# Performance work log

Hardware: AMD Instinct MI355X
Metric: run time of the kernel (lower is better)

Reference implementation:

```python
import jax, jax.numpy as jnp
import numpy as np

C = 2048
EPS = 1e-12


def conv1x1(x, w, b):
    # x: [B,C_in,H,W], w: [C_out,C_in], b: [C_out]
    return jnp.einsum('oc,bchw->bohw', w, x) + b[None, :, None, None]


def unfold3x3(x):
    # torch F.unfold(kernel=3, padding=1): output [B, C*9, H*W],
    # feature order (c, ki, kj) with c slowest.
    B, Cc, H, W = x.shape
    xp = jnp.pad(x, ((0, 0), (0, 0), (1, 1), (1, 1)))
    patches = jnp.stack([xp[:, :, ki:ki + H, kj:kj + W]
                         for ki in range(3) for kj in range(3)], axis=2)  # [B,C,9,H,W]
    return patches.reshape(B, Cc * 9, H * W)


def fold3x3(u, H, W):
    # torch F.fold(kernel=3, padding=1): overlap-add. u: [B, C*9, H*W]
    B = u.shape[0]
    Cc = u.shape[1] // 9
    t = u.reshape(B, Cc, 3, 3, H, W)
    out = jnp.zeros((B, Cc, H + 2, W + 2), dtype=u.dtype)
    for ki in range(3):
        for kj in range(3):
            out = out.at[:, :, ki:ki + H, kj:kj + W].add(t[:, :, ki, kj])
    return out[:, :, 1:1 + H, 1:1 + W]


def l2norm(x, axis):
    n = jnp.sqrt(jnp.sum(x * x, axis=axis, keepdims=True))
    return x / jnp.maximum(n, EPS)


def setup_inputs() -> dict:
    key = jax.random.key(0)
    ks = jax.random.split(key, 8)
    B, H, W = 4, 24, 24
    s = 0.02
    return {
        'part_ref': jax.random.normal(ks[0], (B, C, H, W), jnp.float32),
        'part_target': jax.random.normal(ks[1], (B, C, H, W), jnp.float32),
        'wq': jax.random.normal(ks[2], (C, C), jnp.float32) * s,
        'bq': jnp.zeros((C,), jnp.float32),
        'wk': jax.random.normal(ks[3], (C, C), jnp.float32) * s,
        'bk': jnp.zeros((C,), jnp.float32),
        'wt': jax.random.normal(ks[4], (C, 2 * C), jnp.float32) * s,
        'bt': jnp.zeros((C,), jnp.float32),
    }


def reference(part_ref, part_target, wq, bq, wk, bk, wt, bt):
    B, _, H, W = part_ref.shape
    part_target_o = part_target
    k = conv1x1(part_ref, wk, bk)
    q = conv1x1(part_target, wq, bq)

    tgt_unf = unfold3x3(q)        # [B, C*9, L]
    ref_unf1 = unfold3x3(k)       # [B, C*9, L]

    ref_n = l2norm(jnp.transpose(ref_unf1, (0, 2, 1)), axis=2)  # [B, L, C*9]
    tgt_n = l2norm(tgt_unf, axis=1)                              # [B, C*9, L]

    R = jnp.einsum('blc,bcm->blm', ref_n, tgt_n)  # [B, L_ref, L_tgt]
    R_star = jnp.max(R, axis=1)                   # [B, L]
    R_arg = jnp.argmax(R, axis=1)                 # [B, L]

    # gather best ref patch per target location along dim 2
    T_unf = jnp.take_along_axis(ref_unf1, R_arg[:, None, :], axis=2)  # [B, C*9, L]
    T_part = fold3x3(T_unf, H, W) / 9.0

    S = R_star.reshape(B, 1, H, W)
    x_res = jnp.concatenate((q, T_part), axis=1)  # [B, 2C, H, W]
    res = conv1x1(x_res, wt, bt) * S + part_target_o
    return res
```

## Files before the change

### kernel.cpp

```cpp
#include <hip/hip_runtime.h>
#include <cstddef>
#include <cstdint>

#define LPIX 576
#define CCH  2048
#define NB   4

typedef __attribute__((ext_vector_type(8))) short short8;
typedef __attribute__((ext_vector_type(4))) float f32x4;
typedef __attribute__((ext_vector_type(4))) unsigned short u16x4;

__device__ __forceinline__ unsigned short f2bf(float f) {
    uint32_t u = __builtin_bit_cast(uint32_t, f);
    u += 0x7fff + ((u >> 16) & 1);
    return (unsigned short)(u >> 16);
}
__device__ __forceinline__ float bf2f(unsigned short s) {
    return __builtin_bit_cast(float, (uint32_t)s << 16);
}

__device__ __forceinline__ void gload_lds16(const void* g, void* l) {
    __builtin_amdgcn_global_load_lds((const __attribute__((address_space(1))) void*)g,
                                     (__attribute__((address_space(3))) void*)l, 16, 0, 0);
}

template<int BM, int BN>
__device__ __forceinline__ void mm_core64(
    const short* __restrict__ Ab, int lda,
    const short* __restrict__ Bb, int ldb,
    int k0, int kend, short* As, short* Bs,
    int m0, int n0, f32x4 (&acc)[BM/32][BN/32])
{
    const int tid  = threadIdx.x;
    const int lane = tid & 63;
    const int w    = tid >> 6;
    const int wm = (w & 1) * (BM / 2);
    const int wn = (w >> 1) * (BN / 2);
    const int l15 = lane & 15;
    const int k8  = (lane >> 4) * 8;
    const int r   = tid >> 2;
    const int kk  = (tid & 3) * 8;

    const short* Aptr[BM / 32]; short* Alds[BM / 32];
    #pragma unroll
    for (int u = 0; u < BM / 32; ++u) {
        const int p = u & 1, g = u >> 1;
        Aptr[u] = Ab + (size_t)(m0 + g * 64 + r) * lda + p * 32 + kk;
        Alds[u] = As + p * BM * 32 + g * 2048 + tid * 8;
    }
    const short* Bptr[BN / 32]; short* Blds[BN / 32];
    #pragma unroll
    for (int u = 0; u < BN / 32; ++u) {
        const int p = u & 1, g = u >> 1;
        Bptr[u] = Bb + (size_t)(n0 + g * 64 + r) * ldb + p * 32 + kk;
        Blds[u] = Bs + p * BN * 32 + g * 2048 + tid * 8;
    }

    for (int c0 = k0; c0 < kend; c0 += 64) {
        #pragma unroll
        for (int u = 0; u < BM / 32; ++u) gload_lds16(Aptr[u] + c0, Alds[u]);
        #pragma unroll
        for (int u = 0; u < BN / 32; ++u) gload_lds16(Bptr[u] + c0, Blds[u]);
        __syncthreads();
        #pragma unroll
        for (int s = 0; s < 2; ++s) {
            short8 fa[BM / 32], fb[BN / 32];
            #pragma unroll
            for (int i = 0; i < BM / 32; ++i)
                fa[i] = *(const short8*)(As + s * BM * 32 + (wm + i * 16 + l15) * 32 + k8);
            #pragma unroll
            for (int j = 0; j < BN / 32; ++j)
                fb[j] = *(const short8*)(Bs + s * BN * 32 + (wn + j * 16 + l15) * 32 + k8);
            #pragma unroll
            for (int i = 0; i < BM / 32; ++i)
                #pragma unroll
                for (int j = 0; j < BN / 32; ++j)
                    acc[i][j] = __builtin_amdgcn_mfma_f32_16x16x32_bf16(fa[i], fb[j], acc[i][j], 0, 0, 0);
        }
        __syncthreads();
    }
}

__global__ __launch_bounds__(256) void wcast2_k(const float* __restrict__ wq,
                                                const float* __restrict__ wk,
                                                short* __restrict__ Wb) {
    const float* W = blockIdx.y ? wk : wq;
    short* D = Wb + (size_t)blockIdx.y * CCH * CCH;
    int i = (blockIdx.x * 256 + threadIdx.x) * 4;
    float4 v = *(const float4*)(W + i);
    u16x4 u;
    u.x = f2bf(v.x); u.y = f2bf(v.y); u.z = f2bf(v.z); u.w = f2bf(v.w);
    *(u16x4*)(D + i) = u;
}

__global__ __launch_bounds__(256) void wcast_k(const float* __restrict__ W,
                                               short* __restrict__ Wb) {
    int i = (blockIdx.x * 256 + threadIdx.x) * 4;
    float4 v = *(const float4*)(W + i);
    u16x4 u;
    u.x = f2bf(v.x); u.y = f2bf(v.y); u.z = f2bf(v.z); u.w = f2bf(v.w);
    *(u16x4*)(Wb + i) = u;
}

__global__ __launch_bounds__(256) void tcast_k(const float* __restrict__ tgt,
                                               const float* __restrict__ ref,
                                               short* __restrict__ T1) {
    __shared__ float tile[32][33];
    const int z = blockIdx.z;
    const int b = z & 3, which = z >> 2;
    const float* X = (which ? ref : tgt) + (size_t)b * CCH * LPIX;
    const int c0 = blockIdx.y * 32;
    const int l0 = blockIdx.x * 32;
    const int tx = threadIdx.x, ty = threadIdx.y;
    #pragma unroll
    for (int j = 0; j < 4; ++j)
        tile[ty + j * 8][tx] = X[(size_t)(c0 + ty + j * 8) * LPIX + l0 + tx];
    __syncthreads();
    short* D = T1 + ((size_t)(which * NB + b) * LPIX) * CCH;
    #pragma unroll
    for (int j = 0; j < 4; ++j)
        D[(size_t)(l0 + ty + j * 8) * CCH + c0 + tx] = (short)f2bf(tile[tx][ty + j * 8]);
}

__global__ __launch_bounds__(256) void conv_k(
    const short* __restrict__ T1, const short* __restrict__ Wb,
    const float* __restrict__ bq, const float* __restrict__ bk,
    short* __restrict__ x2t, short* __restrict__ kt,
    float* __restrict__ nq, float* __restrict__ nk)
{
    __shared__ short As[64 * 64];
    __shared__ short Bs[128 * 64];
    const int id = blockIdx.x;
    const int xcd = id & 7, slot = id >> 3;
    const int sid = xcd * 4 + slot / 36;
    const int r36 = slot % 36;
    const int which = sid >> 4;
    const int m0 = (r36 % 9) * 64;
    const int n0 = (sid & 15) * 128;
    const int b  = r36 / 9;
    const short* Ab = T1 + (size_t)(which * NB + b) * LPIX * CCH;
    const short* Bb = Wb + (size_t)which * CCH * CCH;
    const float* bias = which ? bk : bq;
    short* Yb = which ? (kt + (size_t)b * LPIX * CCH) : (x2t + (size_t)b * LPIX * 4096);
    float* Nb = (which ? nk : nq) + b * LPIX;
    const int ldy = which ? CCH : 4096;
    f32x4 acc[2][4] = {};
    mm_core64<64, 128>(Ab, CCH, Bb, CCH, 0, CCH, As, Bs, m0, n0, acc);
    const int lane = threadIdx.x & 63, w = threadIdx.x >> 6;
    const int wm = (w & 1) * 32, wn = (w >> 1) * 64;
    const int l15 = lane & 15, quad = lane >> 4;
    float pv[2][4] = {};
    #pragma unroll
    for (int i = 0; i < 2; ++i)
        #pragma unroll
        for (int j = 0; j < 4; ++j) {
            const int gn = n0 + wn + j * 16 + l15;
            const float bi = bias[gn];
            #pragma unroll
            for (int r = 0; r < 4; ++r) {
                const int gm = m0 + wm + i * 16 + quad * 4 + r;
                float v = acc[i][j][r] + bi;
                pv[i][r] += v * v;
                Yb[(size_t)gm * ldy + gn] = (short)f2bf(v);
            }
        }
    #pragma unroll
    for (int i = 0; i < 2; ++i)
        #pragma unroll
        for (int r = 0; r < 4; ++r) {
            float s = pv[i][r];
            #pragma unroll
            for (int m = 1; m < 16; m <<= 1) s += __shfl_xor(s, m);
            if (l15 == 0) {
                const int gm = m0 + wm + i * 16 + quad * 4 + r;
                atomicAdd(&Nb[gm], s);
            }
        }
}

__global__ __launch_bounds__(256) void gram_k(
    const short* __restrict__ kt, const short* __restrict__ x2t,
    float* __restrict__ Mpart)
{
    __shared__ short As[64 * 64];
    __shared__ short Bs[64 * 64];
    const int z = blockIdx.z;
    const int b = z >> 1, kc = z & 1;
    const short* Ab = kt + (size_t)b * LPIX * CCH;
    const short* Bb = x2t + (size_t)b * LPIX * 4096;
    const int m0 = blockIdx.y * 64;
    const int n0 = blockIdx.x * 64;
    f32x4 acc[2][2] = {};
    mm_core64<64, 64>(Ab, CCH, Bb, 4096, kc * 1024, kc * 1024 + 1024, As, Bs, m0, n0, acc);
    float* Mb = Mpart + (size_t)(kc * NB + b) * LPIX * LPIX;
    const int lane = threadIdx.x & 63, w = threadIdx.x >> 6;
    const int wm = (w & 1) * 32, wn = (w >> 1) * 32;
    const int l15 = lane & 15, quad = lane >> 4;
    #pragma unroll
    for (int i = 0; i < 2; ++i)
        #pragma unroll
        for (int j = 0; j < 2; ++j) {
            const int gn = n0 + wn + j * 16 + l15;
            #pragma unroll
            for (int r = 0; r < 4; ++r) {
                const int gm = m0 + wm + i * 16 + quad * 4 + r;
                Mb[(size_t)gm * LPIX + gn] = acc[i][j][r];
            }
        }
}

__global__ __launch_bounds__(256) void fin_k(
    const short* __restrict__ wtb, const short* __restrict__ x2t,
    const float* __restrict__ bt, const float* __restrict__ S,
    const float* __restrict__ PT, float* __restrict__ out)
{
    __shared__ short As[128 * 64];
    __shared__ short Bs[64 * 64];
    const int id = blockIdx.x;
    const int xcd = id & 7, slot = id >> 3;
    const int hi = slot >= 36;
    const int r36 = slot - hi * 36;
    const int m0 = (xcd * 2 + hi) * 128;
    const int n0 = (r36 % 9) * 64;
    const int b  = r36 / 9;
    const short* Bb = x2t + (size_t)b * LPIX * 4096;
    f32x4 acc[4][2] = {};
    mm_core64<128, 64>(wtb, 4096, Bb, 4096, 0, 4096, As, Bs, m0, n0, acc);
    const int lane = threadIdx.x & 63, w = threadIdx.x >> 6;
    const int wm = (w & 1) * 64, wn = (w >> 1) * 32;
    const int l15 = lane & 15, quad = lane >> 4;
    #pragma unroll
    for (int i = 0; i < 4; ++i)
        #pragma unroll
        for (int j = 0; j < 2; ++j) {
            const int gn = n0 + wn + j * 16 + l15;
            const float sv = S[b * LPIX + gn];
            #pragma unroll
            for (int r = 0; r < 4; ++r) {
                const int gm = m0 + wm + i * 16 + quad * 4 + r;
                float v = (acc[i][j][r] + bt[gm]) * sv
                        + PT[((size_t)b * CCH + gm) * LPIX + gn];
                out[((size_t)b * CCH + gm) * LPIX + gn] = v;
            }
        }
}

__global__ __launch_bounds__(256) void argmax1_k(
    const float* __restrict__ Mpart, const float* __restrict__ nk,
    float* __restrict__ Pv, int* __restrict__ Pi)
{
    const int b   = blockIdx.z;
    const int lrb = blockIdx.y;
    const int tx = threadIdx.x, ty = threadIdx.y;
    const int tid = ty * 64 + tx;
    __shared__ float invNkS[24];
    if (tid < 24) {
        const int jr = tid;
        float s = 0.f;
        #pragma unroll
        for (int di = -1; di <= 1; ++di) {
            const int ii = lrb + di;
            if ((unsigned)ii > 23u) continue;
            #pragma unroll
            for (int dj = -1; dj <= 1; ++dj) {
                const int jj = jr + dj;
                if ((unsigned)jj > 23u) continue;
                s += nk[b * LPIX + ii * 24 + jj];
            }
        }
        invNkS[jr] = 1.0f / fmaxf(sqrtf(s), 1e-12f);
    }
    __syncthreads();
    const int lt = blockIdx.x * 64 + tx;
    const int it = lt / 24, jt = lt % 24;
    const float* Mb0 = Mpart + (size_t)b * LPIX * LPIX;
    const float* Mb1 = Mpart + (size_t)(NB + b) * LPIX * LPIX;
    float best = -1e30f; int bidx = 0;
    #pragma unroll
    for (int i = 0; i < 6; ++i) {
        const int jr = ty + i * 4;
        const int lr = lrb * 24 + jr;
        const int base = lr * LPIX + lt;
        float g = 0.f;
        #pragma unroll
        for (int di = -1; di <= 1; ++di) {
            if ((unsigned)(lrb + di) > 23u || (unsigned)(it + di) > 23u) continue;
            #pragma unroll
            for (int dj = -1; dj <= 1; ++dj) {
                if ((unsigned)(jr + dj) > 23u || (unsigned)(jt + dj) > 23u) continue;
                const int o = base + (di * 24 + dj) * (LPIX + 1);
                g += Mb0[o] + Mb1[o];
            }
        }
        float v = g * invNkS[jr];
        if (v > best) { best = v; bidx = lr; }
    }
    __shared__ float rv[4][64];
    __shared__ int   ri[4][64];
    rv[ty][tx] = best; ri[ty][tx] = bidx;
    __syncthreads();
    if (ty == 0) {
        #pragma unroll
        for (int y = 1; y < 4; ++y) {
            float v = rv[y][tx]; int id = ri[y][tx];
            if (v > best || (v == best && id < bidx)) { best = v; bidx = id; }
        }
        Pv[((size_t)b * 24 + lrb) * LPIX + lt] = best;
        Pi[((size_t)b * 24 + lrb) * LPIX + lt] = bidx;
    }
}

__global__ __launch_bounds__(256) void argmax2_k(
    const float* __restrict__ Pv, const int* __restrict__ Pi,
    const float* __restrict__ nq,
    float* __restrict__ S, int* __restrict__ Arg)
{
    int idx = blockIdx.x * 256 + threadIdx.x;
    if (idx >= NB * LPIX) return;
    int b = idx / LPIX, lt = idx % LPIX;
    int it = lt / 24, jt = lt % 24;
    float s = 0.f;
    #pragma unroll
    for (int di = -1; di <= 1; ++di) {
        const int ii = it + di;
        if ((unsigned)ii > 23u) continue;
        #pragma unroll
        for (int dj = -1; dj <= 1; ++dj) {
            const int jj = jt + dj;
            if ((unsigned)jj > 23u) continue;
            s += nq[b * LPIX + ii * 24 + jj];
        }
    }
    const float invNq = 1.0f / fmaxf(sqrtf(s), 1e-12f);
    float best = -1e30f; int bidx = 0;
    #pragma unroll
    for (int c = 0; c < 24; ++c) {
        float v = Pv[((size_t)b * 24 + c) * LPIX + lt];
        int  id = Pi[((size_t)b * 24 + c) * LPIX + lt];
        if (v > best || (v == best && id < bidx)) { best = v; bidx = id; }
    }
    S[idx]   = best * invNq;
    Arg[idx] = bidx;
}

__global__ __launch_bounds__(256) void gather_k(
    const short* __restrict__ kt, const int* __restrict__ Arg,
    short* __restrict__ x2t)
{
    const int id = blockIdx.x;
    const int xcd = id & 7, slot = id >> 3;
    const int b  = xcd >> 1;
    const int l0 = ((xcd & 1) * 72 + slot) * 4;
    const int lane = threadIdx.x, ty = threadIdx.y;
    const int tid = ty * 64 + lane;
    __shared__ int tap[4][9];
    if (tid < 36) {
        int px = tid / 9, t9 = tid % 9;
        int l = l0 + px;
        int i = l / 24, j = l % 24;
        int ki = t9 / 3, kj = t9 % 3;
        int ip = i + 1 - ki, jp = j + 1 - kj;
        int off = -1;
        if (ip >= 0 && ip < 24 && jp >= 0 && jp < 24) {
            int a = Arg[b * LPIX + ip * 24 + jp];
            int rr = a / 24 + ki - 1;
            int cc = a % 24 + kj - 1;
            if (rr >= 0 && rr < 24 && cc >= 0 && cc < 24) off = rr * 24 + cc;
        }
        tap[px][t9] = off;
    }
    __syncthreads();
    const int l = l0 + ty;
    const short* Kb = kt + (size_t)b * LPIX * CCH;
    short* dst = x2t + ((size_t)b * LPIX + l) * 4096 + CCH;
    int t[9];
    #pragma unroll
    for (int i = 0; i < 9; ++i) t[i] = tap[ty][i];
    const float inv9 = 1.0f / 9.0f;
    #pragma unroll
    for (int j = 0; j < 8; ++j) {
        int c = (lane + j * 64) * 4;
        float s0 = 0.f, s1 = 0.f, s2 = 0.f, s3 = 0.f;
        #pragma unroll
        for (int t9 = 0; t9 < 9; ++t9) {
            int off = t[t9];
            if (off < 0) continue;
            u16x4 u = *(const u16x4*)(Kb + (size_t)off * CCH + c);
            s0 += bf2f(u.x); s1 += bf2f(u.y); s2 += bf2f(u.z); s3 += bf2f(u.w);
        }
        u16x4 o;
        o.x = f2bf(s0 * inv9); o.y = f2bf(s1 * inv9);
        o.z = f2bf(s2 * inv9); o.w = f2bf(s3 * inv9);
        *(u16x4*)(dst + c) = o;
    }
}

extern "C" void kernel_launch(void* const* d_in, const int* in_sizes, int n_in,
                              void* d_out, int out_size, void* d_ws, size_t ws_size,
                              hipStream_t stream) {
    const float* part_ref = (const float*)d_in[0];
    const float* part_tgt = (const float*)d_in[1];
    const float* wq = (const float*)d_in[2];
    const float* bq = (const float*)d_in[3];
    const float* wk = (const float*)d_in[4];
    const float* bk = (const float*)d_in[5];
    const float* wt = (const float*)d_in[6];
    const float* bt = (const float*)d_in[7];
    float* out = (float*)d_out;

    short* wqb2 = (short*)d_ws;
    short* wtb  = wqb2;
    short* T1   = wqb2 + (size_t)2 * CCH * CCH;
    short* kt   = T1 + (size_t)2 * NB * LPIX * CCH;
    short* x2t  = kt + (size_t)NB * LPIX * CCH;
    float* Mpart = (float*)T1;
    float* nk    = (float*)(x2t + (size_t)NB * LPIX * 4096);
    float* nq    = nk + NB * LPIX;
    float* Sbuf  = nq + NB * LPIX;
    int*   Arg   = (int*)(Sbuf + NB * LPIX);
    float* Pv    = (float*)(Arg + NB * LPIX);
    int*   Pi    = (int*)(Pv + (size_t)24 * NB * LPIX);

    hipMemsetAsync(nk, 0, 2 * NB * LPIX * sizeof(float), stream);

    wcast2_k<<<dim3(4096, 2), 256, 0, stream>>>(wq, wk, wqb2);
    tcast_k<<<dim3(18, 64, 8), dim3(32, 8), 0, stream>>>(part_tgt, part_ref, T1);

    conv_k<<<1152, 256, 0, stream>>>(T1, wqb2, bq, bk, x2t, kt, nq, nk);

    gram_k<<<dim3(9, 9, 8), 256, 0, stream>>>(kt, x2t, Mpart);

    argmax1_k<<<dim3(9, 24, NB), dim3(64, 4), 0, stream>>>(Mpart, nk, Pv, Pi);
    argmax2_k<<<9, 256, 0, stream>>>(Pv, Pi, nq, Sbuf, Arg);

    gather_k<<<576, dim3(64, 4), 0, stream>>>(kt, Arg, x2t);

    wcast_k<<<8192, 256, 0, stream>>>(wt, wtb);
    fin_k<<<576, 256, 0, stream>>>(wtb, x2t, bt, Sbuf, part_tgt, out);
}
```

Measured before the change: 356.1 us.

## Switch GEMM core to 32x32 MFMA with double-buffered swizzled LDS

Replaces the shared GEMM core with one built on 32x32x16 bf16 MFMA, using 2 waves per block and a double-buffered LDS pipeline so the next K-slice loads while the current one computes. An XOR swizzle is applied to the LDS layout to reduce bank conflicts. The conv, gram and final kernels are adapted to the new accumulator layout. The final kernel is retiled to fold batch into the N dimension with 64x128 tiles. Fewer threads per block and doubled LDS may reduce latency hiding and occupancy in exchange for higher MFMA efficiency.

```diff
diff --git a/kernel.cpp b/kernel.cpp
--- a/kernel.cpp
+++ b/kernel.cpp
@@ -8,6 +8,7 @@
 
 typedef __attribute__((ext_vector_type(8))) short short8;
 typedef __attribute__((ext_vector_type(4))) float f32x4;
+typedef __attribute__((ext_vector_type(16))) float f32x16;
 typedef __attribute__((ext_vector_type(4))) unsigned short u16x4;
 
 __device__ __forceinline__ unsigned short f2bf(float f) {
@@ -25,61 +26,94 @@
 }
 
 template<int BM, int BN>
-__device__ __forceinline__ void mm_core64(
+__device__ __forceinline__ void mm32_core(
     const short* __restrict__ Ab, int lda,
     const short* __restrict__ Bb, int ldb,
     int k0, int kend, short* As, short* Bs,
-    int m0, int n0, f32x4 (&acc)[BM/32][BN/32])
-{
+    int m0, int n0, f32x16 (&acc)[BM / 32][BN / 64])
+{
+    constexpr int T   = 128;
+    constexpr int NA  = BM * 8 / T;
+    constexpr int NBC = BN * 8 / T;
+    constexpr int ABUF = BM * 64;
+    constexpr int BBUF = BN * 64;
+
     const int tid  = threadIdx.x;
     const int lane = tid & 63;
     const int w    = tid >> 6;
-    const int wm = (w & 1) * (BM / 2);
-    const int wn = (w >> 1) * (BN / 2);
-    const int l15 = lane & 15;
-    const int k8  = (lane >> 4) * 8;
-    const int r   = tid >> 2;
-    const int kk  = (tid & 3) * 8;
-
-    const short* Aptr[BM / 32]; short* Alds[BM / 32];
-    #pragma unroll
-    for (int u = 0; u < BM / 32; ++u) {
-        const int p = u & 1, g = u >> 1;
-        Aptr[u] = Ab + (size_t)(m0 + g * 64 + r) * lda + p * 32 + kk;
-        Alds[u] = As + p * BM * 32 + g * 2048 + tid * 8;
-    }
-    const short* Bptr[BN / 32]; short* Blds[BN / 32];
-    #pragma unroll
-    for (int u = 0; u < BN / 32; ++u) {
-        const int p = u & 1, g = u >> 1;
-        Bptr[u] = Bb + (size_t)(n0 + g * 64 + r) * ldb + p * 32 + kk;
-        Blds[u] = Bs + p * BN * 32 + g * 2048 + tid * 8;
-    }
-
-    for (int c0 = k0; c0 < kend; c0 += 64) {
-        #pragma unroll
-        for (int u = 0; u < BM / 32; ++u) gload_lds16(Aptr[u] + c0, Alds[u]);
-        #pragma unroll
-        for (int u = 0; u < BN / 32; ++u) gload_lds16(Bptr[u] + c0, Blds[u]);
-        __syncthreads();
-        #pragma unroll
-        for (int s = 0; s < 2; ++s) {
-            short8 fa[BM / 32], fb[BN / 32];
-            #pragma unroll
-            for (int i = 0; i < BM / 32; ++i)
-                fa[i] = *(const short8*)(As + s * BM * 32 + (wm + i * 16 + l15) * 32 + k8);
-            #pragma unroll
-            for (int j = 0; j < BN / 32; ++j)
-                fb[j] = *(const short8*)(Bs + s * BN * 32 + (wn + j * 16 + l15) * 32 + k8);
+    const int wn   = w * (BN / 2);
+    const int u31  = lane & 31;
+    const int h    = lane >> 5;
+
+    const short* Aptr[NA]; short* Alds[NA];
+    #pragma unroll
+    for (int t = 0; t < NA; ++t) {
+        const int c   = t * T + tid;
+        const int p   = c / (BM * 4);
+        const int cip = c % (BM * 4);
+        const int row = cip >> 2, q = cip & 3;
+        const int s   = q ^ ((row >> 1) & 3);
+        Aptr[t] = Ab + (size_t)(m0 + row) * lda + p * 32 + s * 8;
+        Alds[t] = As + c * 8;
+    }
+    const short* Bptr[NBC]; short* Blds[NBC];
+    #pragma unroll
+    for (int t = 0; t < NBC; ++t) {
+        const int c   = t * T + tid;
+        const int p   = c / (BN * 4);
+        const int cip = c % (BN * 4);
+        const int row = cip >> 2, q = cip & 3;
+        const int s   = q ^ ((row >> 1) & 3);
+        Bptr[t] = Bb + (size_t)(n0 + row) * ldb + p * 32 + s * 8;
+        Blds[t] = Bs + c * 8;
+    }
+
+    const int nsteps = (kend - k0) >> 6;
+
+    #pragma unroll
+    for (int t = 0; t < NA; ++t)  gload_lds16(Aptr[t] + k0, Alds[t]);
+    #pragma unroll
+    for (int t = 0; t < NBC; ++t) gload_lds16(Bptr[t] + k0, Blds[t]);
+    __syncthreads();
+
+    for (int it = 0; it < nsteps; ++it) {
+        const int cur = it & 1;
+        const short* Ac = As + cur * ABUF;
+        const short* Bc = Bs + cur * BBUF;
+        if (it + 1 < nsteps) {
+            const int c1 = k0 + (it + 1) * 64;
+            const int nb = cur ^ 1;
+            #pragma unroll
+            for (int t = 0; t < NA; ++t)  gload_lds16(Aptr[t] + c1, Alds[t] + nb * ABUF);
+            #pragma unroll
+            for (int t = 0; t < NBC; ++t) gload_lds16(Bptr[t] + c1, Blds[t] + nb * BBUF);
+        }
+        #pragma unroll
+        for (int t4 = 0; t4 < 4; ++t4) {
+            const int p = t4 >> 1;
+            const int s = (t4 & 1) * 2 + h;
+            short8 fa[BM / 32], fb[BN / 64];
+            #pragma unroll
+            for (int i = 0; i < BM / 32; ++i) {
+                const int row = i * 32 + u31;
+                fa[i] = *(const short8*)(Ac + p * BM * 32 + row * 32 + ((s ^ ((row >> 1) & 3)) * 8));
+            }
+            #pragma unroll
+            for (int j = 0; j < BN / 64; ++j) {
+                const int row = wn + j * 32 + u31;
+                fb[j] = *(const short8*)(Bc + p * BN * 32 + row * 32 + ((s ^ ((row >> 1) & 3)) * 8));
+            }
             #pragma unroll
             for (int i = 0; i < BM / 32; ++i)
                 #pragma unroll
-                for (int j = 0; j < BN / 32; ++j)
-                    acc[i][j] = __builtin_amdgcn_mfma_f32_16x16x32_bf16(fa[i], fb[j], acc[i][j], 0, 0, 0);
+                for (int j = 0; j < BN / 64; ++j)
+                    acc[i][j] = __builtin_amdgcn_mfma_f32_32x32x16_bf16(fa[i], fb[j], acc[i][j], 0, 0, 0);
         }
         __syncthreads();
     }
 }
+
+#define ROW32(r, h) (((r) & 3) + 8 * ((r) >> 2) + 4 * (h))
 
 __global__ __launch_bounds__(256) void wcast2_k(const float* __restrict__ wq,
                                                 const float* __restrict__ wk,
@@ -122,14 +156,14 @@
         D[(size_t)(l0 + ty + j * 8) * CCH + c0 + tx] = (short)f2bf(tile[tx][ty + j * 8]);
 }
 
-__global__ __launch_bounds__(256) void conv_k(
+__global__ __launch_bounds__(128) void conv_k(
     const short* __restrict__ T1, const short* __restrict__ Wb,
     const float* __restrict__ bq, const float* __restrict__ bk,
     short* __restrict__ x2t, short* __restrict__ kt,
     float* __restrict__ nq, float* __restrict__ nk)
 {
-    __shared__ short As[64 * 64];
-    __shared__ short Bs[128 * 64];
+    __shared__ short As[2 * 64 * 64];
+    __shared__ short Bs[2 * 128 * 64];
     const int id = blockIdx.x;
     const int xcd = id & 7, slot = id >> 3;
     const int sid = xcd * 4 + slot / 36;
@@ -144,103 +178,100 @@
     short* Yb = which ? (kt + (size_t)b * LPIX * CCH) : (x2t + (size_t)b * LPIX * 4096);
     float* Nb = (which ? nk : nq) + b * LPIX;
     const int ldy = which ? CCH : 4096;
-    f32x4 acc[2][4] = {};
-    mm_core64<64, 128>(Ab, CCH, Bb, CCH, 0, CCH, As, Bs, m0, n0, acc);
+
+    f32x16 acc[2][2] = {};
+    mm32_core<64, 128>(Ab, CCH, Bb, CCH, 0, CCH, As, Bs, m0, n0, acc);
+
     const int lane = threadIdx.x & 63, w = threadIdx.x >> 6;
-    const int wm = (w & 1) * 32, wn = (w >> 1) * 64;
-    const int l15 = lane & 15, quad = lane >> 4;
-    float pv[2][4] = {};
-    #pragma unroll
-    for (int i = 0; i < 2; ++i)
-        #pragma unroll
-        for (int j = 0; j < 4; ++j) {
-            const int gn = n0 + wn + j * 16 + l15;
+    const int wn = w * 64, u31 = lane & 31, h = lane >> 5;
+    #pragma unroll
+    for (int i = 0; i < 2; ++i) {
+        float pv[16];
+        #pragma unroll
+        for (int r = 0; r < 16; ++r) pv[r] = 0.f;
+        #pragma unroll
+        for (int j = 0; j < 2; ++j) {
+            const int gn = n0 + wn + j * 32 + u31;
             const float bi = bias[gn];
             #pragma unroll
-            for (int r = 0; r < 4; ++r) {
-                const int gm = m0 + wm + i * 16 + quad * 4 + r;
+            for (int r = 0; r < 16; ++r) {
+                const int gm = m0 + i * 32 + ROW32(r, h);
                 float v = acc[i][j][r] + bi;
-                pv[i][r] += v * v;
+                pv[r] += v * v;
                 Yb[(size_t)gm * ldy + gn] = (short)f2bf(v);
             }
         }
-    #pragma unroll
-    for (int i = 0; i < 2; ++i)
-        #pragma unroll
-        for (int r = 0; r < 4; ++r) {
-            float s = pv[i][r];
-            #pragma unroll
-            for (int m = 1; m < 16; m <<= 1) s += __shfl_xor(s, m);
-            if (l15 == 0) {
-                const int gm = m0 + wm + i * 16 + quad * 4 + r;
+        #pragma unroll
+        for (int r = 0; r < 16; ++r) {
+            float s = pv[r];
+            #pragma unroll
+            for (int m = 1; m < 32; m <<= 1) s += __shfl_xor(s, m);
+            if (u31 == 0) {
+                const int gm = m0 + i * 32 + ROW32(r, h);
                 atomicAdd(&Nb[gm], s);
             }
         }
-}
-
-__global__ __launch_bounds__(256) void gram_k(
+    }
+}
+
+__global__ __launch_bounds__(128) void gram_k(
     const short* __restrict__ kt, const short* __restrict__ x2t,
     float* __restrict__ Mpart)
 {
-    __shared__ short As[64 * 64];
-    __shared__ short Bs[64 * 64];
+    __shared__ short As[2 * 64 * 64];
+    __shared__ short Bs[2 * 64 * 64];
     const int z = blockIdx.z;
     const int b = z >> 1, kc = z & 1;
     const short* Ab = kt + (size_t)b * LPIX * CCH;
     const short* Bb = x2t + (size_t)b * LPIX * 4096;
     const int m0 = blockIdx.y * 64;
     const int n0 = blockIdx.x * 64;
-    f32x4 acc[2][2] = {};
-    mm_core64<64, 64>(Ab, CCH, Bb, 4096, kc * 1024, kc * 1024 + 1024, As, Bs, m0, n0, acc);
+    f32x16 acc[2][1] = {};
+    mm32_core<64, 64>(Ab, CCH, Bb, 4096, kc * 1024, kc * 1024 + 1024, As, Bs, m0, n0, acc);
     float* Mb = Mpart + (size_t)(kc * NB + b) * LPIX * LPIX;
     const int lane = threadIdx.x & 63, w = threadIdx.x >> 6;
-    const int wm = (w & 1) * 32, wn = (w >> 1) * 32;
-    const int l15 = lane & 15, quad = lane >> 4;
-    #pragma unroll
-    for (int i = 0; i < 2; ++i)
-        #pragma unroll
-        for (int j = 0; j < 2; ++j) {
-            const int gn = n0 + wn + j * 16 + l15;
-            #pragma unroll
-            for (int r = 0; r < 4; ++r) {
-                const int gm = m0 + wm + i * 16 + quad * 4 + r;
-                Mb[(size_t)gm * LPIX + gn] = acc[i][j][r];
-            }
-        }
-}
-
-__global__ __launch_bounds__(256) void fin_k(
+    const int wn = w * 32, u31 = lane & 31, h = lane >> 5;
+    #pragma unroll
+    for (int i = 0; i < 2; ++i) {
+        const int gn = n0 + wn + u31;
+        #pragma unroll
+        for (int r = 0; r < 16; ++r) {
+            const int gm = m0 + i * 32 + ROW32(r, h);
+            Mb[(size_t)gm * LPIX + gn] = acc[i][0][r];
+        }
+    }
+}
+
+__global__ __launch_bounds__(128) void fin_k(
     const short* __restrict__ wtb, const short* __restrict__ x2t,
     const float* __restrict__ bt, const float* __restrict__ S,
     const float* __restrict__ PT, float* __restrict__ out)
 {
-    __shared__ short As[128 * 64];
-    __shared__ short Bs[64 * 64];
+    __shared__ short As[2 * 64 * 64];
+    __shared__ short Bs[2 * 128 * 64];
     const int id = blockIdx.x;
     const int xcd = id & 7, slot = id >> 3;
-    const int hi = slot >= 36;
-    const int r36 = slot - hi * 36;
-    const int m0 = (xcd * 2 + hi) * 128;
-    const int n0 = (r36 % 9) * 64;
-    const int b  = r36 / 9;
-    const short* Bb = x2t + (size_t)b * LPIX * 4096;
-    f32x4 acc[4][2] = {};
-    mm_core64<128, 64>(wtb, 4096, Bb, 4096, 0, 4096, As, Bs, m0, n0, acc);
+    const int sid = xcd * 4 + slot / 18;
+    const int m0 = sid * 64;
+    const int n0 = (slot % 18) * 128;
+    f32x16 acc[2][2] = {};
+    mm32_core<64, 128>(wtb, 4096, x2t, 4096, 0, 4096, As, Bs, m0, n0, acc);
     const int lane = threadIdx.x & 63, w = threadIdx.x >> 6;
-    const int wm = (w & 1) * 64, wn = (w >> 1) * 32;
-    const int l15 = lane & 15, quad = lane >> 4;
-    #pragma unroll
-    for (int i = 0; i < 4; ++i)
+    const int wn = w * 64, u31 = lane & 31, h = lane >> 5;
+    #pragma unroll
+    for (int i = 0; i < 2; ++i)
         #pragma unroll
         for (int j = 0; j < 2; ++j) {
-            const int gn = n0 + wn + j * 16 + l15;
-            const float sv = S[b * LPIX + gn];
-            #pragma unroll
-            for (int r = 0; r < 4; ++r) {
-                const int gm = m0 + wm + i * 16 + quad * 4 + r;
+            const int gn = n0 + wn + j * 32 + u31;
+            const int bb = gn / LPIX;
+            const int l  = gn - bb * LPIX;
+            const float sv = S[gn];
+            #pragma unroll
+            for (int r = 0; r < 16; ++r) {
+                const int gm = m0 + i * 32 + ROW32(r, h);
                 float v = (acc[i][j][r] + bt[gm]) * sv
-                        + PT[((size_t)b * CCH + gm) * LPIX + gn];
-                out[((size_t)b * CCH + gm) * LPIX + gn] = v;
+                        + PT[((size_t)bb * CCH + gm) * LPIX + l];
+                out[((size_t)bb * CCH + gm) * LPIX + l] = v;
             }
         }
 }
@@ -426,9 +457,9 @@
     wcast2_k<<<dim3(4096, 2), 256, 0, stream>>>(wq, wk, wqb2);
     tcast_k<<<dim3(18, 64, 8), dim3(32, 8), 0, stream>>>(part_tgt, part_ref, T1);
 
-    conv_k<<<1152, 256, 0, stream>>>(T1, wqb2, bq, bk, x2t, kt, nq, nk);
-
-    gram_k<<<dim3(9, 9, 8), 256, 0, stream>>>(kt, x2t, Mpart);
+    conv_k<<<1152, 128, 0, stream>>>(T1, wqb2, bq, bk, x2t, kt, nq, nk);
+
+    gram_k<<<dim3(9, 9, 8), 128, 0, stream>>>(kt, x2t, Mpart);
 
     argmax1_k<<<dim3(9, 24, NB), dim3(64, 4), 0, stream>>>(Mpart, nk, Pv, Pi);
     argmax2_k<<<9, 256, 0, stream>>>(Pv, Pi, nq, Sbuf, Arg);
@@ -436,5 +467,5 @@
     gather_k<<<576, dim3(64, 4), 0, stream>>>(kt, Arg, x2t);
 
     wcast_k<<<8192, 256, 0, stream>>>(wt, wtb);
-    fin_k<<<576, 256, 0, stream>>>(wtb, x2t, bt, Sbuf, part_tgt, out);
-}
+    fin_k<<<576, 128, 0, stream>>>(wtb, x2t, bt, Sbuf, part_tgt, out);
+}
```

Result: slower. 411.2 us (+15.5%).
